# Performance work log

Measured on AMD Instinct MI355X. Metric: run time of the kernel, lower is better.

## Reference

```python
import jax, jax.numpy as jnp
import numpy as np
import math

D_MODEL = 1024
N_HEADS = 8
D_FF = 4 * D_MODEL
EPS = 1e-5


def layer_norm(x, g, b):
    mu = jnp.mean(x, axis=-1, keepdims=True)
    var = jnp.mean(jnp.square(x - mu), axis=-1, keepdims=True)
    return (x - mu) / jnp.sqrt(var + EPS) * g + b


def setup_inputs() -> dict:
    key = jax.random.key(0)
    ks = jax.random.split(key, 8)
    B, S = 1, 4096
    x = jax.random.normal(ks[0], (B, S, D_MODEL), dtype=jnp.float32)
    # linear params (stored as [in, out]); init scale ~ 1/sqrt(fan_in)
    qkv_w = jax.random.normal(ks[1], (D_MODEL, 3 * D_MODEL), dtype=jnp.float32) * (1.0 / math.sqrt(D_MODEL))
    qkv_b = jnp.zeros((3 * D_MODEL,), dtype=jnp.float32)
    w1 = jax.random.normal(ks[2], (D_MODEL, D_FF), dtype=jnp.float32) * (1.0 / math.sqrt(D_MODEL))
    b1 = jnp.zeros((D_FF,), dtype=jnp.float32)
    w2 = jax.random.normal(ks[3], (D_FF, D_MODEL), dtype=jnp.float32) * (1.0 / math.sqrt(D_FF))
    b2 = jnp.zeros((D_MODEL,), dtype=jnp.float32)
    ln1_g = jnp.ones((D_MODEL,), dtype=jnp.float32)
    ln1_b = jnp.zeros((D_MODEL,), dtype=jnp.float32)
    ln2_g = jnp.ones((D_MODEL,), dtype=jnp.float32)
    ln2_b = jnp.zeros((D_MODEL,), dtype=jnp.float32)
    return {"x": x, "ln1_g": ln1_g, "ln1_b": ln1_b, "qkv_w": qkv_w, "qkv_b": qkv_b,
            "ln2_g": ln2_g, "ln2_b": ln2_b, "w1": w1, "b1": b1, "w2": w2, "b2": b2}


def reference(x, ln1_g, ln1_b, qkv_w, qkv_b, ln2_g, ln2_b, w1, b1, w2, b2):
    B, S, D = x.shape
    hd = D // N_HEADS
    scaler = math.sqrt(hd)

    h = layer_norm(x, ln1_g, ln1_b)                       # [B,S,D]
    qkv = h @ qkv_w + qkv_b                               # [B,S,3D]
    q, k, v = jnp.split(qkv, 3, axis=-1)
    # b s (h d) -> b h s d
    def split_heads(t):
        return t.reshape(B, S, N_HEADS, hd).transpose(0, 2, 1, 3)
    q, k, v = split_heads(q), split_heads(k), split_heads(v)
    scores = jnp.einsum('bhqd,bhkd->bhqk', q, k) / scaler  # [B,H,S,S] materialized, as in source
    attn = jax.nn.softmax(scores, axis=-1)
    heads = jnp.einsum('bhqk,bhkd->bhqd', attn, v)        # [B,H,S,hd]
    attn_score = heads.transpose(0, 2, 1, 3).reshape(B, S, D)  # b h t d -> b t (h d)
    # NOTE: source returns attn_score (the proj Linear output is discarded)
    h = attn_score + h                                     # residual with ln1 output
    h = layer_norm(h, ln2_g, ln2_b)
    h = jax.nn.gelu(h @ w1 + b1, approximate=False) @ w2 + b2  # no final residual
    return h
```

## Files before the change

### kernel.cpp

```cpp
#include <hip/hip_runtime.h>
#include <stdint.h>


typedef __bf16 bf16;
typedef __attribute__((ext_vector_type(8))) __bf16 bf16x8;
typedef __attribute__((ext_vector_type(4))) __bf16 bf16x4;
typedef __attribute__((ext_vector_type(4))) float f32x4;

#define DEV static __device__ __forceinline__

#define QSCALE 0.12751741687f

DEV void gload_lds16(const void* gsrc, void* ldst) {
  typedef const __attribute__((address_space(1))) uint32_t gq_t;
  typedef __attribute__((address_space(3))) uint32_t lq_t;
  __builtin_amdgcn_global_load_lds((gq_t*)(uintptr_t)gsrc, (lq_t*)(uintptr_t)ldst,
                                   16, 0, 0);
}

DEV f32x4 mfma16(bf16x8 a, bf16x8 b, f32x4 c) {
  return __builtin_amdgcn_mfma_f32_16x16x32_bf16(a, b, c, 0, 0, 0);
}

__global__ __launch_bounds__(256) void ln1_kernel(
    const float* __restrict__ x, const float* __restrict__ gw,
    const float* __restrict__ bw, bf16* __restrict__ out) {
  int row = blockIdx.x, t = threadIdx.x;
  const float* xr = x + (size_t)row * 1024;
  f32x4 v = *(const f32x4*)(xr + t * 4);
  float s = v[0] + v[1] + v[2] + v[3];
  float s2 = v[0] * v[0] + v[1] * v[1] + v[2] * v[2] + v[3] * v[3];
#pragma unroll
  for (int off = 1; off < 64; off <<= 1) {
    s += __shfl_xor(s, off);
    s2 += __shfl_xor(s2, off);
  }
  __shared__ float red[8];
  if ((t & 63) == 0) { red[t >> 6] = s; red[4 + (t >> 6)] = s2; }
  __syncthreads();
  s = red[0] + red[1] + red[2] + red[3];
  s2 = red[4] + red[5] + red[6] + red[7];
  float mu = s * (1.f / 1024.f);
  float rstd = rsqrtf(s2 * (1.f / 1024.f) - mu * mu + 1e-5f);
  f32x4 gv = *(const f32x4*)(gw + t * 4);
  f32x4 bv = *(const f32x4*)(bw + t * 4);
  bf16x4 o;
#pragma unroll
  for (int j = 0; j < 4; j++) o[j] = (bf16)((v[j] - mu) * rstd * gv[j] + bv[j]);
  *(bf16x4*)(out + (size_t)row * 1024 + t * 4) = o;
}

__global__ __launch_bounds__(256) void resid_ln2_kernel(
    const bf16* __restrict__ Op, const float* __restrict__ lbuf,
    const bf16* __restrict__ h, const float* __restrict__ gw,
    const float* __restrict__ bw, bf16* __restrict__ out) {
  int row = blockIdx.x, t = threadIdx.x;
  int head = t >> 5;
  float l = 0.f;
  float acc[4] = {0.f, 0.f, 0.f, 0.f};
#pragma unroll
  for (int z = 0; z < 4; z++) {
    l += lbuf[(size_t)(z * 8 + head) * 4096 + row];
    bf16x4 ov = *(const bf16x4*)(Op + (size_t)z * 4096 * 1024 +
                                 (size_t)row * 1024 + t * 4);
#pragma unroll
    for (int j = 0; j < 4; j++) acc[j] += (float)ov[j];
  }
  float rl = 1.0f / l;
  bf16x4 hv = *(const bf16x4*)(h + (size_t)row * 1024 + t * 4);
  float vv[4];
#pragma unroll
  for (int j = 0; j < 4; j++) vv[j] = acc[j] * rl + (float)hv[j];
  float s = vv[0] + vv[1] + vv[2] + vv[3];
  float s2 = vv[0] * vv[0] + vv[1] * vv[1] + vv[2] * vv[2] + vv[3] * vv[3];
#pragma unroll
  for (int off = 1; off < 64; off <<= 1) {
    s += __shfl_xor(s, off);
    s2 += __shfl_xor(s2, off);
  }
  __shared__ float red[8];
  if ((t & 63) == 0) { red[t >> 6] = s; red[4 + (t >> 6)] = s2; }
  __syncthreads();
  s = red[0] + red[1] + red[2] + red[3];
  s2 = red[4] + red[5] + red[6] + red[7];
  float mu = s * (1.f / 1024.f);
  float rstd = rsqrtf(s2 * (1.f / 1024.f) - mu * mu + 1e-5f);
  f32x4 gv = *(const f32x4*)(gw + t * 4);
  f32x4 bv = *(const f32x4*)(bw + t * 4);
  bf16x4 o;
#pragma unroll
  for (int j = 0; j < 4; j++) o[j] = (bf16)((vv[j] - mu) * rstd * gv[j] + bv[j]);
  *(bf16x4*)(out + (size_t)row * 1024 + t * 4) = o;
}

__global__ __launch_bounds__(256) void transpose_f32_bf16(
    const float* __restrict__ in, bf16* __restrict__ out, int R, int C) {
  __shared__ float tile[32][33];
  int c0 = blockIdx.x * 32, r0 = blockIdx.y * 32;
  int tx = threadIdx.x & 31, ty = threadIdx.x >> 5;
#pragma unroll
  for (int j = 0; j < 4; j++)
    tile[ty + 8 * j][tx] = in[(size_t)(r0 + ty + 8 * j) * C + c0 + tx];
  __syncthreads();
#pragma unroll
  for (int j = 0; j < 4; j++)
    out[(size_t)(c0 + ty + 8 * j) * R + r0 + tx] = (bf16)tile[tx][ty + 8 * j];
}

template <int EPILOG>
__global__ __launch_bounds__(512) void gemm8p_kernel(
    const bf16* __restrict__ A, const bf16* __restrict__ Bt,
    const float* __restrict__ bias, bf16* __restrict__ Cout,
    bf16* __restrict__ Vout, int M, int N, int K) {
  extern __shared__ char smem[];
  int nwg = gridDim.x * gridDim.y;
  int bid = blockIdx.y * gridDim.x + blockIdx.x;
  int swz = (bid & 7) * (nwg >> 3) + (bid >> 3);
  int bx = swz % gridDim.x, by = swz / gridDim.x;
  int m0 = by * 256, n0 = bx * 256;
  int tid = threadIdx.x, wave = tid >> 6, lane = tid & 63;
  int lr = lane & 15, lg = lane >> 4;
  int wr = (wave >> 2) * 128;
  int wc = (wave & 3) * 64;
  const int NT = K >> 6;

  f32x4 acc[8][4] = {};

  const int sArow = tid >> 3;
  const int scbA = ((tid & 7) * 16) ^ (((tid >> 3) & 7) << 4);
  const int scbB = ((lane & 7) * 16) ^ ((lane >> 3) << 4);

  auto stageA = [&](int c, int T) {
    char* sAb = smem + (size_t)(T & 1) * 32768;
#pragma unroll
    for (int j = 0; j < 2; j++) {
      int r0 = j * 128 + 64 * c;
      gload_lds16(A + (size_t)(m0 + r0 + sArow) * K + T * 64 + scbA / 2,
                  sAb + r0 * 128 + wave * 1024);
    }
  };
  auto stageB = [&](int c, int T) {
    char* sBb = smem + 65536 + (size_t)(T & 1) * 32768;
    int wrun = (wave >> 2) * 64 + 32 * c + (wave & 3) * 8;
#pragma unroll
    for (int j = 0; j < 2; j++) {
      int r0 = j * 128 + wrun;
      gload_lds16(Bt + (size_t)(n0 + r0 + (lane >> 3)) * K + T * 64 + scbB / 2,
                  sBb + r0 * 128);
    }
  };
  auto ldA = [&](bf16x8 (&af)[4][2], int qm, int b) {
    const char* sAb = smem + (size_t)b * 32768;
#pragma unroll
    for (int mm = 0; mm < 4; mm++)
#pragma unroll
      for (int kk = 0; kk < 2; kk++) {
        int rl = wr + 64 * qm + mm * 16 + lr;
        int db = (kk * 64 + lg * 16) ^ ((rl & 7) << 4);
        af[mm][kk] = *(const bf16x8*)(sAb + rl * 128 + db);
      }
  };
  auto ldB = [&](bf16x8 (&bfv)[2][2], int qn, int b) {
    const char* sBb = smem + 65536 + (size_t)b * 32768;
#pragma unroll
    for (int nn = 0; nn < 2; nn++)
#pragma unroll
      for (int kk = 0; kk < 2; kk++) {
        int rb = wc + 32 * qn + nn * 16 + lr;
        int db = (kk * 64 + lg * 16) ^ ((rb & 7) << 4);
        bfv[nn][kk] = *(const bf16x8*)(sBb + rb * 128 + db);
      }
  };
  auto mfmaQ = [&](bf16x8 (&af)[4][2], bf16x8 (&bfv)[2][2], int qm, int qn) {
    __builtin_amdgcn_s_setprio(1);
#pragma unroll
    for (int kk = 0; kk < 2; kk++)
#pragma unroll
      for (int mm = 0; mm < 4; mm++)
#pragma unroll
        for (int nn = 0; nn < 2; nn++)
          acc[qm * 4 + mm][qn * 2 + nn] =
              mfma16(af[mm][kk], bfv[nn][kk], acc[qm * 4 + mm][qn * 2 + nn]);
    __builtin_amdgcn_s_setprio(0);
  };

  stageA(0, 0); stageB(0, 0); stageA(1, 0); stageB(1, 0);
  stageA(0, 1); stageB(0, 1);
  asm volatile("s_waitcnt vmcnt(4)" ::: "memory");
  __builtin_amdgcn_s_barrier();

  for (int T = 0; T < NT; T++) {
    int b = T & 1;
    bf16x8 af[4][2], bfv[2][2];
    ldA(af, 0, b); ldB(bfv, 0, b);
    if (T + 1 < NT) stageA(1, T + 1);
    __builtin_amdgcn_s_barrier();
    mfmaQ(af, bfv, 0, 0);
    __builtin_amdgcn_s_barrier();
    ldB(bfv, 1, b);
    if (T + 1 < NT) stageB(1, T + 1);
    __builtin_amdgcn_s_barrier();
    mfmaQ(af, bfv, 0, 1);
    __builtin_amdgcn_s_barrier();
    ldA(af, 1, b); ldB(bfv, 0, b);
    if (T + 2 < NT) stageA(0, T + 2);
    __builtin_amdgcn_s_barrier();
    mfmaQ(af, bfv, 1, 0);
    __builtin_amdgcn_s_barrier();
    ldB(bfv, 1, b);
    if (T + 2 < NT) stageB(0, T + 2);
    __builtin_amdgcn_s_barrier();
    mfmaQ(af, bfv, 1, 1);
    if (T < NT - 2) asm volatile("s_waitcnt vmcnt(4)" ::: "memory");
    else            asm volatile("s_waitcnt vmcnt(0)" ::: "memory");
    __builtin_amdgcn_s_barrier();
  }

#pragma unroll
  for (int n = 0; n < 4; n++) {
    int col = n0 + wc + n * 16 + lr;
    float bs = bias[col];
#pragma unroll
    for (int m = 0; m < 8; m++) {
      int row0 = m0 + wr + m * 16 + lg * 4;
      if constexpr (EPILOG == 3) {
        if (col >= 2048) {
          bf16x4 pk;
#pragma unroll
          for (int r = 0; r < 4; r++) pk[r] = (bf16)(acc[m][n][r] + bs);
          *(bf16x4*)(Vout + (size_t)(col - 2048) * 4096 + row0) = pk;
          continue;
        }
      }
#pragma unroll
      for (int r = 0; r < 4; r++) {
        float v = acc[m][n][r] + bs;
        if constexpr (EPILOG == 1) {
          float u = v + 0.044715f * v * v * v;
          float e = __builtin_amdgcn_exp2f(-2.3021144f * u);
          v = v / (1.0f + e);
        }
        if constexpr (EPILOG == 3) { if (col < 1024) v *= QSCALE; }
        Cout[(size_t)(row0 + r) * N + col] = (bf16)v;
      }
    }
  }
}

__global__ __launch_bounds__(256) void gemm_ffn2_kernel(
    const bf16* __restrict__ A, const bf16* __restrict__ Bt,
    const float* __restrict__ bias, float* __restrict__ Cout,
    int M, int N, int K) {
  __shared__ bf16 sA[64 * 64];
  __shared__ bf16 sB[128 * 64];
  int nwg = gridDim.x * gridDim.y;
  int bid = blockIdx.y * gridDim.x + blockIdx.x;
  int swz = (bid & 7) * (nwg >> 3) + (bid >> 3);
  int bx = swz % gridDim.x, by = swz / gridDim.x;
  int m0 = by * 64, n0 = bx * 128;
  int tid = threadIdx.x;
  int wave = tid >> 6, lane = tid & 63;
  int lr = lane & 15, lg = lane >> 4;
  int wr = (wave >> 1) * 32, wc = (wave & 1) * 64;

  f32x4 acc[2][4] = {};

  int srow = tid >> 3;
  int scol = (tid & 7) * 8;
  const bf16* Abase = A + (size_t)(m0 + srow) * K + scol;
  const bf16* Bbase = Bt + (size_t)(n0 + srow) * K + scol;

  for (int kt = 0; kt < K; kt += 64) {
#pragma unroll
    for (int i = 0; i < 2; i++)
      gload_lds16(Abase + (size_t)(i * 32) * K + kt,
                  (char*)sA + i * 4096 + wave * 1024);
#pragma unroll
    for (int i = 0; i < 4; i++)
      gload_lds16(Bbase + (size_t)(i * 32) * K + kt,
                  (char*)sB + i * 4096 + wave * 1024);
    __syncthreads();
    bf16x8 af[2][2], bfv[4][2];
#pragma unroll
    for (int m = 0; m < 2; m++)
#pragma unroll
      for (int kk = 0; kk < 2; kk++)
        af[m][kk] = *(const bf16x8*)&sA[(wr + m * 16 + lr) * 64 + kk * 32 + lg * 8];
#pragma unroll
    for (int n = 0; n < 4; n++)
#pragma unroll
      for (int kk = 0; kk < 2; kk++)
        bfv[n][kk] = *(const bf16x8*)&sB[(wc + n * 16 + lr) * 64 + kk * 32 + lg * 8];
#pragma unroll
    for (int kk = 0; kk < 2; kk++)
#pragma unroll
      for (int m = 0; m < 2; m++)
#pragma unroll
        for (int n = 0; n < 4; n++)
          acc[m][n] = mfma16(af[m][kk], bfv[n][kk], acc[m][n]);
    __syncthreads();
  }

#pragma unroll
  for (int n = 0; n < 4; n++) {
    int col = n0 + wc + n * 16 + lr;
    float bs = bias[col];
#pragma unroll
    for (int m = 0; m < 2; m++) {
#pragma unroll
      for (int r = 0; r < 4; r++) {
        int row = m0 + wr + m * 16 + lg * 4 + r;
        Cout[(size_t)row * N + col] = acc[m][n][r] + bs;
      }
    }
  }
}

__global__ __launch_bounds__(256) void attn_kernel(
    const bf16* __restrict__ qkv, const bf16* __restrict__ vt,
    bf16* __restrict__ opart, float* __restrict__ lbuf) {
  constexpr int S = 4096, C3 = 3072;
  __shared__ bf16 sK[64 * 128];
  __shared__ bf16 sV[128 * 64];
  __shared__ bf16 sP[4 * 32 * 64];
  int hh = blockIdx.y;
  int q0 = blockIdx.x * 128;
  int z = blockIdx.z;
  int kv_begin = z * (S / 4), kv_end = kv_begin + (S / 4);
  bf16* obuf = opart + (size_t)z * 4096 * 1024;
  int tid = threadIdx.x, wave = tid >> 6, lane = tid & 63;
  int lr = lane & 15, lg = lane >> 4;

  bf16x8 qf[2][4];
#pragma unroll
  for (int qs = 0; qs < 2; qs++) {
    const bf16* qrow =
        qkv + (size_t)(q0 + wave * 32 + qs * 16 + lr) * C3 + hh * 128 + lg * 8;
#pragma unroll
    for (int kk = 0; kk < 4; kk++) qf[qs][kk] = *(const bf16x8*)(qrow + kk * 32);
  }
  f32x4 o[2][8] = {};
  float lsum[2] = {0.f, 0.f};

  const int krow_s = tid >> 4;
  const int kcb = (tid & 15) * 16;
  const int scbK = kcb ^ ((krow_s & 7) << 4);
  const int vrow_s = tid >> 3;
  const int vcb = (tid & 7) * 16;
  const int scbV = vcb ^ ((vrow_s & 7) << 4);

  const bf16* kbase = qkv + 1024 + hh * 128 + scbK / 2;
  const bf16* vbase = vt + (size_t)(hh * 128 + vrow_s) * S + scbV / 2;

  for (int kv0 = kv_begin; kv0 < kv_end; kv0 += 64) {
#pragma unroll
    for (int i = 0; i < 4; i++)
      gload_lds16(kbase + (size_t)(kv0 + i * 16 + krow_s) * C3,
                  (char*)sK + i * 4096 + wave * 1024);
#pragma unroll
    for (int i = 0; i < 4; i++)
      gload_lds16(vbase + (size_t)(i * 32) * S + kv0,
                  (char*)sV + i * 4096 + wave * 1024);
    __syncthreads();

    char* pw = (char*)sP + wave * 4096;

#pragma unroll
    for (int nf = 0; nf < 4; nf++) {
      f32x4 sc0 = {0.f, 0.f, 0.f, 0.f}, sc1 = sc0;
      __builtin_amdgcn_s_setprio(1);
#pragma unroll
      for (int kk = 0; kk < 4; kk++) {
        int krow = nf * 16 + lr;
        int db = (kk * 64 + lg * 16) ^ ((krow & 7) << 4);
        bf16x8 kf = *(const bf16x8*)((const char*)sK + krow * 256 + db);
        sc0 = mfma16(kf, qf[0][kk], sc0);
        sc1 = mfma16(kf, qf[1][kk], sc1);
      }
      __builtin_amdgcn_s_setprio(0);
      f32x4 scs[2] = {sc0, sc1};
#pragma unroll
      for (int qs = 0; qs < 2; qs++) {
        float p0 = __builtin_amdgcn_exp2f(scs[qs][0]);
        float p1 = __builtin_amdgcn_exp2f(scs[qs][1]);
        float p2 = __builtin_amdgcn_exp2f(scs[qs][2]);
        float p3 = __builtin_amdgcn_exp2f(scs[qs][3]);
        lsum[qs] += (p0 + p1) + (p2 + p3);
        bf16x4 pk;
        pk[0] = (bf16)p0; pk[1] = (bf16)p1; pk[2] = (bf16)p2; pk[3] = (bf16)p3;
        *(bf16x4*)(pw + (qs * 16 + lr) * 128 +
                   ((nf * 32 + lg * 8) ^ ((lr & 7) << 4))) = pk;
      }
    }

    bf16x8 pa[2][2];
#pragma unroll
    for (int qs = 0; qs < 2; qs++)
#pragma unroll
      for (int kk = 0; kk < 2; kk++) {
        int db = (kk * 64 + lg * 16) ^ ((lr & 7) << 4);
        pa[qs][kk] = *(const bf16x8*)(pw + (qs * 16 + lr) * 128 + db);
      }
    __builtin_amdgcn_s_setprio(1);
#pragma unroll
    for (int df = 0; df < 8; df++) {
#pragma unroll
      for (int kk = 0; kk < 2; kk++) {
        int vrow = df * 16 + lr;
        int db = (kk * 64 + lg * 16) ^ ((vrow & 7) << 4);
        bf16x8 vf = *(const bf16x8*)((const char*)sV + vrow * 128 + db);
        o[0][df] = mfma16(pa[0][kk], vf, o[0][df]);
        o[1][df] = mfma16(pa[1][kk], vf, o[1][df]);
      }
    }
    __builtin_amdgcn_s_setprio(0);
    __syncthreads();
  }

#pragma unroll
  for (int qs = 0; qs < 2; qs++) {
    float ls = lsum[qs];
    ls += __shfl_xor(ls, 16);
    ls += __shfl_xor(ls, 32);
    if (lg == 0)
      lbuf[(size_t)(z * 8 + hh) * 4096 + q0 + wave * 32 + qs * 16 + lr] = ls;
#pragma unroll
    for (int df = 0; df < 8; df++) {
      int col = hh * 128 + df * 16 + lr;
#pragma unroll
      for (int r = 0; r < 4; r++) {
        int row = q0 + wave * 32 + qs * 16 + lg * 4 + r;
        obuf[(size_t)row * 1024 + col] = (bf16)o[qs][df][r];
      }
    }
  }
}

extern "C" void kernel_launch(void* const* d_in, const int* in_sizes, int n_in,
                              void* d_out, int out_size, void* d_ws, size_t ws_size,
                              hipStream_t stream) {
  const float* x     = (const float*)d_in[0];
  const float* ln1_g = (const float*)d_in[1];
  const float* ln1_b = (const float*)d_in[2];
  const float* qkv_w = (const float*)d_in[3];
  const float* qkv_b = (const float*)d_in[4];
  const float* ln2_g = (const float*)d_in[5];
  const float* ln2_b = (const float*)d_in[6];
  const float* w1    = (const float*)d_in[7];
  const float* b1    = (const float*)d_in[8];
  const float* w2    = (const float*)d_in[9];
  const float* b2    = (const float*)d_in[10];

  char* ws = (char*)d_ws;
  const size_t MB = 1ull << 20;
  bf16*  h    = (bf16*)(ws + 0);
  bf16*  qkv  = (bf16*)(ws + 8 * MB);
  bf16*  h2   = (bf16*)(ws + 8 * MB);
  bf16*  w1T  = (bf16*)(ws + 16 * MB);
  bf16*  w2T  = (bf16*)(ws + 24 * MB);
  bf16*  vt   = (bf16*)(ws + 32 * MB);
  bf16*  Op   = (bf16*)(ws + 40 * MB);
  bf16*  ffn1 = (bf16*)(ws + 40 * MB);
  float* lbuf = (float*)(ws + 72 * MB);
  bf16*  wTq  = (bf16*)(ws + 72 * MB + 512 * 1024);
  float* outp = (float*)d_out;

  hipFuncSetAttribute(reinterpret_cast<const void*>(gemm8p_kernel<3>),
                      hipFuncAttributeMaxDynamicSharedMemorySize, 131072);
  hipFuncSetAttribute(reinterpret_cast<const void*>(gemm8p_kernel<1>),
                      hipFuncAttributeMaxDynamicSharedMemorySize, 131072);

  ln1_kernel<<<4096, 256, 0, stream>>>(x, ln1_g, ln1_b, h);
  transpose_f32_bf16<<<dim3(3072 / 32, 1024 / 32), 256, 0, stream>>>(qkv_w, wTq, 1024, 3072);
  gemm8p_kernel<3><<<dim3(3072 / 256, 4096 / 256), 512, 131072, stream>>>(
      h, wTq, qkv_b, qkv, vt, 4096, 3072, 1024);
  attn_kernel<<<dim3(32, 8, 4), 256, 0, stream>>>(qkv, vt, Op, lbuf);
  transpose_f32_bf16<<<dim3(4096 / 32, 1024 / 32), 256, 0, stream>>>(w1, w1T, 1024, 4096);
  transpose_f32_bf16<<<dim3(1024 / 32, 4096 / 32), 256, 0, stream>>>(w2, w2T, 4096, 1024);
  resid_ln2_kernel<<<4096, 256, 0, stream>>>(Op, lbuf, h, ln2_g, ln2_b, h2);
  gemm8p_kernel<1><<<dim3(4096 / 256, 4096 / 256), 512, 131072, stream>>>(
      h2, w1T, b1, ffn1, nullptr, 4096, 4096, 1024);
  gemm_ffn2_kernel<<<dim3(1024 / 128, 4096 / 64), 256, 0, stream>>>(
      ffn1, w2T, b2, outp, 4096, 1024, 4096);
}
```

Before: 266.6 us.

## Run FFN2 GEMM as split-K on pipelined 256x256 kernel plus combine pass

Replaces the simple single-buffered FFN2 GEMM with the double-buffered 256x256 gemm8p kernel. K is split four ways across blockIdx.z so the grid still fills the GPU, writing bf16 partial sums that a new combine kernel adds together with the bias into the fp32 output. This targets the low MFMA efficiency of the old 64x128 unpipelined kernel. The cost is an extra 32 MB of partial-sum traffic and one more launch, and rounding partials to bf16 loses some precision. Workspace buffers are re-aliased to hold the partials.

New measurement: 249.9 us. 1.07x faster.

```diff
diff --git a/kernel.cpp b/kernel.cpp
--- a/kernel.cpp
+++ b/kernel.cpp
@@ -93,6 +93,25 @@
   *(bf16x4*)(out + (size_t)row * 1024 + t * 4) = o;
 }
 
+__global__ __launch_bounds__(256) void ffn2_combine_kernel(
+    const bf16* __restrict__ P, const float* __restrict__ b2,
+    float* __restrict__ out) {
+  int row = blockIdx.x, t = threadIdx.x;
+  float acc[4];
+  f32x4 bv = *(const f32x4*)(b2 + t * 4);
+#pragma unroll
+  for (int j = 0; j < 4; j++) acc[j] = bv[j];
+#pragma unroll
+  for (int z = 0; z < 4; z++) {
+    bf16x4 pv = *(const bf16x4*)(P + (size_t)z * 4096 * 1024 +
+                                 (size_t)row * 1024 + t * 4);
+#pragma unroll
+    for (int j = 0; j < 4; j++) acc[j] += (float)pv[j];
+  }
+  f32x4 o = {acc[0], acc[1], acc[2], acc[3]};
+  *(f32x4*)(out + (size_t)row * 1024 + t * 4) = o;
+}
+
 __global__ __launch_bounds__(256) void transpose_f32_bf16(
     const float* __restrict__ in, bf16* __restrict__ out, int R, int C) {
   __shared__ float tile[32][33];
@@ -111,8 +130,13 @@
 __global__ __launch_bounds__(512) void gemm8p_kernel(
     const bf16* __restrict__ A, const bf16* __restrict__ Bt,
     const float* __restrict__ bias, bf16* __restrict__ Cout,
-    bf16* __restrict__ Vout, int M, int N, int K) {
+    bf16* __restrict__ Vout, int M, int N, int K, int Ks) {
   extern __shared__ char smem[];
+  if constexpr (EPILOG == 4) {
+    size_t zo = (size_t)blockIdx.z * Ks;
+    A += zo; Bt += zo;
+    Cout += (size_t)blockIdx.z * ((size_t)M * N);
+  }
   int nwg = gridDim.x * gridDim.y;
   int bid = blockIdx.y * gridDim.x + blockIdx.x;
   int swz = (bid & 7) * (nwg >> 3) + (bid >> 3);
@@ -122,7 +146,7 @@
   int lr = lane & 15, lg = lane >> 4;
   int wr = (wave >> 2) * 128;
   int wc = (wave & 3) * 64;
-  const int NT = K >> 6;
+  const int NT = Ks >> 6;
 
   f32x4 acc[8][4] = {};
 
@@ -219,7 +243,7 @@
 #pragma unroll
   for (int n = 0; n < 4; n++) {
     int col = n0 + wc + n * 16 + lr;
-    float bs = bias[col];
+    float bs = (EPILOG == 4) ? 0.f : bias[col];
 #pragma unroll
     for (int m = 0; m < 8; m++) {
       int row0 = m0 + wr + m * 16 + lg * 4;
@@ -242,75 +266,6 @@
         }
         if constexpr (EPILOG == 3) { if (col < 1024) v *= QSCALE; }
         Cout[(size_t)(row0 + r) * N + col] = (bf16)v;
-      }
-    }
-  }
-}
-
-__global__ __launch_bounds__(256) void gemm_ffn2_kernel(
-    const bf16* __restrict__ A, const bf16* __restrict__ Bt,
-    const float* __restrict__ bias, float* __restrict__ Cout,
-    int M, int N, int K) {
-  __shared__ bf16 sA[64 * 64];
-  __shared__ bf16 sB[128 * 64];
-  int nwg = gridDim.x * gridDim.y;
-  int bid = blockIdx.y * gridDim.x + blockIdx.x;
-  int swz = (bid & 7) * (nwg >> 3) + (bid >> 3);
-  int bx = swz % gridDim.x, by = swz / gridDim.x;
-  int m0 = by * 64, n0 = bx * 128;
-  int tid = threadIdx.x;
-  int wave = tid >> 6, lane = tid & 63;
-  int lr = lane & 15, lg = lane >> 4;
-  int wr = (wave >> 1) * 32, wc = (wave & 1) * 64;
-
-  f32x4 acc[2][4] = {};
-
-  int srow = tid >> 3;
-  int scol = (tid & 7) * 8;
-  const bf16* Abase = A + (size_t)(m0 + srow) * K + scol;
-  const bf16* Bbase = Bt + (size_t)(n0 + srow) * K + scol;
-
-  for (int kt = 0; kt < K; kt += 64) {
-#pragma unroll
-    for (int i = 0; i < 2; i++)
-      gload_lds16(Abase + (size_t)(i * 32) * K + kt,
-                  (char*)sA + i * 4096 + wave * 1024);
-#pragma unroll
-    for (int i = 0; i < 4; i++)
-      gload_lds16(Bbase + (size_t)(i * 32) * K + kt,
-                  (char*)sB + i * 4096 + wave * 1024);
-    __syncthreads();
-    bf16x8 af[2][2], bfv[4][2];
-#pragma unroll
-    for (int m = 0; m < 2; m++)
-#pragma unroll
-      for (int kk = 0; kk < 2; kk++)
-        af[m][kk] = *(const bf16x8*)&sA[(wr + m * 16 + lr) * 64 + kk * 32 + lg * 8];
-#pragma unroll
-    for (int n = 0; n < 4; n++)
-#pragma unroll
-      for (int kk = 0; kk < 2; kk++)
-        bfv[n][kk] = *(const bf16x8*)&sB[(wc + n * 16 + lr) * 64 + kk * 32 + lg * 8];
-#pragma unroll
-    for (int kk = 0; kk < 2; kk++)
-#pragma unroll
-      for (int m = 0; m < 2; m++)
-#pragma unroll
-        for (int n = 0; n < 4; n++)
-          acc[m][n] = mfma16(af[m][kk], bfv[n][kk], acc[m][n]);
-    __syncthreads();
-  }
-
-#pragma unroll
-  for (int n = 0; n < 4; n++) {
-    int col = n0 + wc + n * 16 + lr;
-    float bs = bias[col];
-#pragma unroll
-    for (int m = 0; m < 2; m++) {
-#pragma unroll
-      for (int r = 0; r < 4; r++) {
-        int row = m0 + wr + m * 16 + lg * 4 + r;
-        Cout[(size_t)row * N + col] = acc[m][n][r] + bs;
       }
     }
   }
@@ -453,33 +408,37 @@
 
   char* ws = (char*)d_ws;
   const size_t MB = 1ull << 20;
-  bf16*  h    = (bf16*)(ws + 0);
-  bf16*  qkv  = (bf16*)(ws + 8 * MB);
-  bf16*  h2   = (bf16*)(ws + 8 * MB);
-  bf16*  w1T  = (bf16*)(ws + 16 * MB);
-  bf16*  w2T  = (bf16*)(ws + 24 * MB);
-  bf16*  vt   = (bf16*)(ws + 32 * MB);
-  bf16*  Op   = (bf16*)(ws + 40 * MB);
-  bf16*  ffn1 = (bf16*)(ws + 40 * MB);
-  float* lbuf = (float*)(ws + 72 * MB);
-  bf16*  wTq  = (bf16*)(ws + 72 * MB + 512 * 1024);
-  float* outp = (float*)d_out;
+  bf16*  h     = (bf16*)(ws + 0);
+  bf16*  qkv   = (bf16*)(ws + 8 * MB);
+  bf16*  h2    = (bf16*)(ws + 8 * MB);
+  bf16*  w1T   = (bf16*)(ws + 16 * MB);
+  bf16*  fpart = (bf16*)(ws + 0);
+  bf16*  vt    = (bf16*)(ws + 32 * MB);
+  bf16*  w2T   = (bf16*)(ws + 32 * MB);
+  bf16*  Op    = (bf16*)(ws + 40 * MB);
+  bf16*  ffn1  = (bf16*)(ws + 40 * MB);
+  float* lbuf  = (float*)(ws + 72 * MB);
+  bf16*  wTq   = (bf16*)(ws + 72 * MB + 512 * 1024);
+  float* outp  = (float*)d_out;
 
   hipFuncSetAttribute(reinterpret_cast<const void*>(gemm8p_kernel<3>),
                       hipFuncAttributeMaxDynamicSharedMemorySize, 131072);
   hipFuncSetAttribute(reinterpret_cast<const void*>(gemm8p_kernel<1>),
                       hipFuncAttributeMaxDynamicSharedMemorySize, 131072);
+  hipFuncSetAttribute(reinterpret_cast<const void*>(gemm8p_kernel<4>),
+                      hipFuncAttributeMaxDynamicSharedMemorySize, 131072);
 
   ln1_kernel<<<4096, 256, 0, stream>>>(x, ln1_g, ln1_b, h);
   transpose_f32_bf16<<<dim3(3072 / 32, 1024 / 32), 256, 0, stream>>>(qkv_w, wTq, 1024, 3072);
   gemm8p_kernel<3><<<dim3(3072 / 256, 4096 / 256), 512, 131072, stream>>>(
-      h, wTq, qkv_b, qkv, vt, 4096, 3072, 1024);
+      h, wTq, qkv_b, qkv, vt, 4096, 3072, 1024, 1024);
   attn_kernel<<<dim3(32, 8, 4), 256, 0, stream>>>(qkv, vt, Op, lbuf);
   transpose_f32_bf16<<<dim3(4096 / 32, 1024 / 32), 256, 0, stream>>>(w1, w1T, 1024, 4096);
   transpose_f32_bf16<<<dim3(1024 / 32, 4096 / 32), 256, 0, stream>>>(w2, w2T, 4096, 1024);
   resid_ln2_kernel<<<4096, 256, 0, stream>>>(Op, lbuf, h, ln2_g, ln2_b, h2);
   gemm8p_kernel<1><<<dim3(4096 / 256, 4096 / 256), 512, 131072, stream>>>(
-      h2, w1T, b1, ffn1, nullptr, 4096, 4096, 1024);
-  gemm_ffn2_kernel<<<dim3(1024 / 128, 4096 / 64), 256, 0, stream>>>(
-      ffn1, w2T, b2, outp, 4096, 1024, 4096);
-}
+      h2, w1T, b1, ffn1, nullptr, 4096, 4096, 1024, 1024);
+  gemm8p_kernel<4><<<dim3(1024 / 256, 4096 / 256, 4), 512, 131072, stream>>>(
+      ffn1, w2T, nullptr, fpart, nullptr, 4096, 1024, 4096, 1024);
+  ffn2_combine_kernel<<<4096, 256, 0, stream>>>(fpart, b2, outp);
+}
```
